# Performance work log

Measured on AMD Instinct MI355X. Metric: run time of the kernel, lower is better.

## Reference

```python
import jax, jax.numpy as jnp
import numpy as np
import math

L, C, H, FF, V, T, B = 12, 768, 12, 3072, 50257, 512, 4
D = C // H  # head dim = 64


def _layernorm(x, w, b, eps=1e-5):
    m = x.mean(-1, keepdims=True)
    v = ((x - m) ** 2).mean(-1, keepdims=True)
    return (x - m) / jnp.sqrt(v + eps) * w + b


def _gelu(x):
    # tanh-approximate GELU exactly as in the torch module
    return 0.5 * x * (1.0 + jnp.tanh(math.sqrt(2.0 / math.pi) * (x + 0.044715 * x ** 3)))


def setup_inputs() -> dict:
    key = jax.random.key(0)
    ks = jax.random.split(key, 12)
    std = 0.02
    proj_std = 0.02 / math.sqrt(2 * L)
    inp = {
        "idx": jax.random.randint(ks[0], (B, T), 0, V),
        "targets": jax.random.randint(ks[1], (B, T), 0, V),
        "wte": jax.random.normal(ks[2], (V, C), jnp.float32) * std,
        "wpe": jax.random.normal(ks[3], (T, C), jnp.float32) * std,
        "ln1_w": jnp.ones((L, C), jnp.float32),
        "ln1_b": jnp.zeros((L, C), jnp.float32),
        "attn_w": jax.random.normal(ks[4], (L, C, 3 * C), jnp.float32) * std,
        "attn_b": jnp.zeros((L, 3 * C), jnp.float32),
        "attnp_w": jax.random.normal(ks[5], (L, C, C), jnp.float32) * proj_std,
        "attnp_b": jnp.zeros((L, C), jnp.float32),
        "ln2_w": jnp.ones((L, C), jnp.float32),
        "ln2_b": jnp.zeros((L, C), jnp.float32),
        "fc_w": jax.random.normal(ks[6], (L, C, FF), jnp.float32) * std,
        "fc_b": jnp.zeros((L, FF), jnp.float32),
        "fcp_w": jax.random.normal(ks[7], (L, FF, C), jnp.float32) * proj_std,
        "fcp_b": jnp.zeros((L, C), jnp.float32),
        "lnf_w": jnp.ones((C,), jnp.float32),
        "lnf_b": jnp.zeros((C,), jnp.float32),
        "lm_w": jax.random.normal(ks[8], (C, V), jnp.float32) * std,  # lm_head.weight.T
    }
    return inp


def _gpt_forward(idx, targets, wte, wpe, ln1_w, ln1_b, attn_w, attn_b,
                 attnp_w, attnp_b, ln2_w, ln2_b, fc_w, fc_b, fcp_w, fcp_b,
                 lnf_w, lnf_b, lm_w):
    b, t = idx.shape
    x = wte[idx] + wpe[:t][None]  # [B,T,C]
    causal = jnp.tril(jnp.ones((t, t), bool))  # [T,T]
    neg_inf = jnp.float32(-jnp.inf)

    def block(x, p):
        l1w, l1b, aw, ab, pw, pb, l2w, l2b, fw, fb, qw, qb = p
        h = _layernorm(x, l1w, l1b)
        qkv = h @ aw + ab  # [B,T,3C]
        q, k, v = jnp.split(qkv, 3, axis=-1)
        q = q.reshape(b, t, H, D).transpose(0, 2, 1, 3)  # [B,H,T,D]
        k = k.reshape(b, t, H, D).transpose(0, 2, 1, 3)
        v = v.reshape(b, t, H, D).transpose(0, 2, 1, 3)
        att = jnp.einsum('bhqd,bhkd->bhqk', q, k) * (1.0 / math.sqrt(D))
        att = jnp.where(causal, att, neg_inf)
        att = jax.nn.softmax(att, axis=-1)
        y = jnp.einsum('bhqk,bhkd->bhqd', att, v)  # [B,H,T,D]
        y = y.transpose(0, 2, 1, 3).reshape(b, t, C)
        x = x + (y @ pw + pb)
        h2 = _layernorm(x, l2w, l2b)
        x = x + (_gelu(h2 @ fw + fb) @ qw + qb)
        return x, None

    params = (ln1_w, ln1_b, attn_w, attn_b, attnp_w, attnp_b,
              ln2_w, ln2_b, fc_w, fc_b, fcp_w, fcp_b)
    x, _ = jax.lax.scan(block, x, params)
    x = _layernorm(x, lnf_w, lnf_b)
    logits = x @ lm_w  # [B,T,V]

    # cross_entropy with ignore_index=-100
    logp = jax.nn.log_softmax(logits, axis=-1)
    tgt = targets.reshape(-1)
    valid = (tgt != -100)
    safe_tgt = jnp.where(valid, tgt, 0)
    nll = -jnp.take_along_axis(logp.reshape(-1, logits.shape[-1]),
                               safe_tgt[:, None], axis=1)[:, 0]
    loss = jnp.sum(nll * valid) / jnp.maximum(jnp.sum(valid), 1)
    return logits, loss


def reference(idx, targets, wte, wpe, ln1_w, ln1_b, attn_w, attn_b,
              attnp_w, attnp_b, ln2_w, ln2_b, fc_w, fc_b, fcp_w, fcp_b,
              lnf_w, lnf_b, lm_w):
    return _gpt_forward(idx, targets, wte, wpe, ln1_w, ln1_b, attn_w, attn_b,
                        attnp_w, attnp_b, ln2_w, ln2_b, fc_w, fc_b,
                        fcp_w, fcp_b, lnf_w, lnf_b, lm_w)
```

## Files before the change

kernel.cpp:

```cpp
#include <hip/hip_runtime.h>
#include <hip/hip_bf16.h>
#include <math.h>

#define L_ 12
#define C_ 768
#define H_ 12
#define FF_ 3072
#define V_ 50257
#define VP2_ 50432
#define T_ 512
#define B_ 4
#define D_ 64
#define M_ (B_*T_)
#define BH_ (B_*H_)
#define NPAN_LM 197

typedef __attribute__((ext_vector_type(8))) short short8;
typedef __attribute__((ext_vector_type(4))) float f32x4;
typedef __attribute__((ext_vector_type(8))) unsigned short us8;

__device__ __forceinline__ float bf2f(unsigned short u) {
    return __uint_as_float(((unsigned)u) << 16);
}
__device__ __forceinline__ unsigned short f2bf(float f) {
    unsigned u = __float_as_uint(f);
    unsigned r = u + 0x7fff + ((u >> 16) & 1);
    return (unsigned short)(r >> 16);
}

__device__ __forceinline__ void transpose_tile(
    const float* __restrict__ W, __hip_bfloat16* __restrict__ WT,
    int K, int N, int Npad, int bx, int by, int bz)
{
    __shared__ float tile[64][65];
    const float* Wl = W + (size_t)bz * K * N;
    __hip_bfloat16* WTl = WT + (size_t)bz * Npad * K;
    int k0 = by * 64, n0 = bx * 64;
    int tid = threadIdx.x;
    int tn = tid & 63, tk4 = tid >> 6;
#pragma unroll 4
    for (int i = 0; i < 16; ++i) {
        int k = tk4 * 16 + i;
        int n = n0 + tn;
        tile[k][tn] = (n < N) ? Wl[(size_t)(k0 + k) * N + n] : 0.f;
    }
    __syncthreads();
#pragma unroll
    for (int i = 0; i < 2; ++i) {
        int p = tid + i * 256;
        int n = p >> 3;
        int k8 = (p & 7) * 8;
        us8 v;
#pragma unroll
        for (int e = 0; e < 8; ++e) v[e] = f2bf(tile[k8 + e][n]);
        *(us8*)((unsigned short*)WTl + (size_t)(n0 + n) * K + k0 + k8) = v;
    }
}

__global__ __launch_bounds__(256) void transpose_all_kernel(
    const float* W0, __hip_bfloat16* T0,
    const float* W1, __hip_bfloat16* T1,
    const float* W2, __hip_bfloat16* T2,
    const float* W3, __hip_bfloat16* T3,
    const float* W4, __hip_bfloat16* T4)
{
    int bid = blockIdx.x;
    if (bid < 5184) {
        int bx = bid % 36, r = bid / 36;
        transpose_tile(W0, T0, C_, 3 * C_, 3 * C_, bx, r % 12, r / 12);
    } else if (bid < 6912) {
        int lb = bid - 5184;
        int bx = lb % 12, r = lb / 12;
        transpose_tile(W1, T1, C_, C_, C_, bx, r % 12, r / 12);
    } else if (bid < 13824) {
        int lb = bid - 6912;
        int bx = lb % 48, r = lb / 48;
        transpose_tile(W2, T2, C_, FF_, FF_, bx, r % 12, r / 12);
    } else if (bid < 20736) {
        int lb = bid - 13824;
        int bx = lb % 12, r = lb / 12;
        transpose_tile(W3, T3, FF_, C_, C_, bx, r % 48, r / 48);
    } else {
        int lb = bid - 20736;
        int bx = lb % 788, by = lb / 788;
        transpose_tile(W4, T4, C_, V_, VP2_, bx, by, 0);
    }
}

__global__ void embed_kernel(const int* __restrict__ idx, const float* __restrict__ wte,
                             const float* __restrict__ wpe, float* __restrict__ x, int total)
{
    int i = blockIdx.x * blockDim.x + threadIdx.x;
    if (i >= total) return;
    int c = i % C_;
    int row = i / C_;
    int t = row % T_;
    x[i] = wte[(size_t)idx[row] * C_ + c] + wpe[(size_t)t * C_ + c];
}

__global__ __launch_bounds__(256) void layernorm_kernel(
    const float* __restrict__ x, const float* __restrict__ w, const float* __restrict__ b,
    __hip_bfloat16* __restrict__ out)
{
    int row = blockIdx.x;
    int tid = threadIdx.x;
    const float* xr = x + (size_t)row * C_;
    float lx[3];
    float s = 0.f;
#pragma unroll
    for (int i = 0; i < 3; ++i) { lx[i] = xr[tid + i * 256]; s += lx[i]; }
    __shared__ float red[4];
    for (int off = 32; off > 0; off >>= 1) s += __shfl_down(s, off, 64);
    if ((tid & 63) == 0) red[tid >> 6] = s;
    __syncthreads();
    if (tid == 0) red[0] = red[0] + red[1] + red[2] + red[3];
    __syncthreads();
    float mean = red[0] * (1.f / (float)C_);
    __syncthreads();
    float v = 0.f;
#pragma unroll
    for (int i = 0; i < 3; ++i) { float d = lx[i] - mean; v += d * d; }
    for (int off = 32; off > 0; off >>= 1) v += __shfl_down(v, off, 64);
    if ((tid & 63) == 0) red[tid >> 6] = v;
    __syncthreads();
    if (tid == 0) red[0] = red[0] + red[1] + red[2] + red[3];
    __syncthreads();
    float rstd = rsqrtf(red[0] * (1.f / (float)C_) + 1e-5f);
#pragma unroll
    for (int i = 0; i < 3; ++i) {
        int c = tid + i * 256;
        ((unsigned short*)out)[(size_t)row * C_ + c] = f2bf((lx[i] - mean) * rstd * w[c] + b[c]);
    }
}

template<int MT, int NT, int WM, int WN, int BUFS, int SPLITK,
         int OUTBF, int GELU, int RESID, int LOSSP, int QKVPACK, int ATOMIC>
__global__ __launch_bounds__(64 * WM * WN) void mfma_gemm(
    const __hip_bfloat16* __restrict__ A,
    const __hip_bfloat16* __restrict__ Bt,
    const float* __restrict__ bias,
    const float* __restrict__ resid,
    void* __restrict__ Cout,
    int M, int N, int K, int NB,
    float* __restrict__ lpart, int NPAN,
    unsigned short* __restrict__ Qp, unsigned short* __restrict__ Kp,
    unsigned short* __restrict__ Vt)
{
    constexpr int NTHREADS = 64 * WM * WN;
    constexpr int MPAN = M_ / MT;
    constexpr int MFR = MT / (16 * WM);
    constexpr int AL = (MT * 4) / NTHREADS;
    constexpr int BL = (NT * 4) / NTHREADS;
    constexpr int LOADS = AL + BL;

    int nwg = NB * MPAN * SPLITK;
    int orig = blockIdx.x;
    int xcd = orig & 7;
    int q = nwg >> 3, rr_ = nwg & 7;
    int wgid = (xcd < rr_ ? xcd * (q + 1) : rr_ * (q + 1) + (xcd - rr_) * q) + (orig >> 3);
    int chunk = wgid / (NB * MPAN);
    int rem = wgid % (NB * MPAN);
    int npan = rem / MPAN, mpan = rem % MPAN;
    int m0 = mpan * MT, n0 = npan * NT;
    int KC = K / SPLITK;
    int kbase = chunk * KC;

    __shared__ __hip_bfloat16 As[BUFS][MT * 32];
    __shared__ __hip_bfloat16 Bs[BUFS][NT * 32];
    __shared__ float Lsum[WN][LOSSP ? MT : 1];
    int tid = threadIdx.x;
    int lane = tid & 63, w = tid >> 6;
    int wn = w % WN, wm = w / WN;
    int lrow = lane & 15, g = lane >> 4;
    f32x4 acc[MFR][4] = {};

    const __hip_bfloat16* Ab = A + (size_t)m0 * K + kbase;
    const __hip_bfloat16* Bb = Bt + (size_t)n0 * K + kbase;

    auto stage = [&](int buf, int k0) {
#pragma unroll
        for (int i = 0; i < AL; ++i) {
            int c = tid + i * NTHREADS;
            int row = c >> 2, s = c & 3;
            int l = (s - (row >> 1)) & 3;
            __builtin_amdgcn_global_load_lds(
                (const __attribute__((address_space(1))) void*)(Ab + (size_t)row * K + k0 + l * 8),
                (__attribute__((address_space(3))) void*)(&As[buf][c * 8]), 16, 0, 0);
        }
#pragma unroll
        for (int i = 0; i < BL; ++i) {
            int c = tid + i * NTHREADS;
            int row = c >> 2, s = c & 3;
            int l = (s - (row >> 1)) & 3;
            __builtin_amdgcn_global_load_lds(
                (const __attribute__((address_space(1))) void*)(Bb + (size_t)row * K + k0 + l * 8),
                (__attribute__((address_space(3))) void*)(&Bs[buf][c * 8]), 16, 0, 0);
        }
    };
    auto do_tile = [&](int buf) {
        short8 a[MFR], b[4];
#pragma unroll
        for (int i = 0; i < MFR; ++i) {
            int row = wm * (MT / WM) + i * 16 + lrow;
            int s = (g + (row >> 1)) & 3;
            a[i] = *(const short8*)&As[buf][row * 32 + s * 8];
        }
#pragma unroll
        for (int j = 0; j < 4; ++j) {
            int row = wn * 64 + j * 16 + lrow;
            int s = (g + (row >> 1)) & 3;
            b[j] = *(const short8*)&Bs[buf][row * 32 + s * 8];
        }
        asm volatile("s_waitcnt lgkmcnt(0)" ::: "memory");
        __builtin_amdgcn_sched_barrier(0);
        __builtin_amdgcn_s_setprio(1);
#pragma unroll
        for (int i = 0; i < MFR; ++i)
#pragma unroll
            for (int j = 0; j < 4; ++j)
                acc[i][j] = __builtin_amdgcn_mfma_f32_16x16x32_bf16(a[i], b[j], acc[i][j], 0, 0, 0);
        __builtin_amdgcn_s_setprio(0);
    };

    int nk = KC >> 5;
#pragma unroll
    for (int i = 0; i < BUFS - 1; ++i) stage(i, i << 5);
    for (int t = 0; t < nk; ++t) {
        int ahead = nk - 1 - t;
        if (ahead > BUFS - 2) ahead = BUFS - 2;
        if (ahead == 1) {
            if constexpr (LOADS == 3) asm volatile("s_waitcnt vmcnt(3)" ::: "memory");
            else                      asm volatile("s_waitcnt vmcnt(4)" ::: "memory");
        } else if (ahead >= 2) {
            if constexpr (LOADS == 3) asm volatile("s_waitcnt vmcnt(6)" ::: "memory");
            else                      asm volatile("s_waitcnt vmcnt(8)" ::: "memory");
        } else {
            asm volatile("s_waitcnt vmcnt(0)" ::: "memory");
        }
        __builtin_amdgcn_s_barrier();
        if (t + BUFS - 1 < nk) stage((t + BUFS - 1) % BUFS, (t + BUFS - 1) << 5);
        do_tile(t % BUFS);
    }

    int r0 = g * 4;
#pragma unroll
    for (int i = 0; i < MFR; ++i) {
#pragma unroll
        for (int j = 0; j < 4; ++j) {
            int col = n0 + wn * 64 + j * 16 + lrow;
            if (col >= N) continue;
            float bv = (bias && (SPLITK == 1 || chunk == 0)) ? bias[col] : 0.f;
#pragma unroll
            for (int r = 0; r < 4; ++r) {
                int row = m0 + wm * (MT / WM) + i * 16 + r0 + r;
                float v = acc[i][j][r] + bv;
                if (GELU) {
                    float t = 0.7978845608028654f * (v + 0.044715f * v * v * v);
                    v = 0.5f * v * (1.f + tanhf(t));
                }
                if (RESID) v += resid[(size_t)row * N + col];
                if (ATOMIC) {
                    atomicAdd(&((float*)Cout)[(size_t)row * N + col], v);
                } else if (QKVPACK) {
                    int bb = row >> 9, tt = row & (T_ - 1);
                    int which = col / 768;
                    int cc = col - which * 768;
                    int hh = cc >> 6, d = cc & 63;
                    size_t bh = (size_t)bb * H_ + hh;
                    unsigned short u = f2bf(v);
                    if (which == 0)      Qp[(bh * T_ + tt) * 64 + d] = u;
                    else if (which == 1) Kp[(bh * T_ + tt) * 64 + d] = u;
                    else                 Vt[(bh * 64 + d) * T_ + tt] = u;
                } else if (OUTBF) {
                    ((unsigned short*)Cout)[(size_t)row * N + col] = f2bf(v);
                } else {
                    ((float*)Cout)[(size_t)row * N + col] = v;
                }
            }
        }
    }
    if (LOSSP) {
#pragma unroll
        for (int i = 0; i < MFR; ++i) {
#pragma unroll
            for (int r = 0; r < 4; ++r) {
                float ss = 0.f;
#pragma unroll
                for (int j = 0; j < 4; ++j) {
                    int col = n0 + wn * 64 + j * 16 + lrow;
                    if (col < V_) ss += __expf(acc[i][j][r]);
                }
#pragma unroll
                for (int d2 = 1; d2 < 16; d2 <<= 1) ss += __shfl_xor(ss, d2, 64);
                if ((lane & 15) == 0) {
                    int rloc = wm * (MT / WM) + i * 16 + g * 4 + r;
                    Lsum[wn][rloc] = ss;
                }
            }
        }
        __syncthreads();
        if (tid < MT) {
            float ss = Lsum[0][tid];
#pragma unroll
            for (int ww = 1; ww < WN; ++ww) ss += Lsum[ww][tid];
            lpart[(size_t)(m0 + tid) * NPAN + npan] = ss;
        }
    }
}

__global__ __launch_bounds__(256) void flash_attn_kernel(
    const unsigned short* __restrict__ Qp, const unsigned short* __restrict__ Kp,
    const unsigned short* __restrict__ Vt, unsigned short* __restrict__ y)
{
    int bid = blockIdx.x;
    int xcd = bid & 7;
    int s_ = bid >> 3;
    int bh = xcd * 6 + (s_ % 6);
    int qg = 7 - s_ / 6;
    int b = bh / H_, h = bh % H_;
    int tid = threadIdx.x;
    int w = tid >> 6;
    int lane = tid & 63;
    int c = lane & 15, g = lane >> 4;
    int q0 = (qg * 4 + w) * 16;

    const unsigned short* Qb = Qp + ((size_t)bh * T_ + q0) * 64;
    const unsigned short* Kb = Kp + (size_t)bh * T_ * 64;
    const unsigned short* Vb = Vt + (size_t)bh * 64 * T_;

    short8 qf0 = *(const short8*)(Qb + (size_t)c * 64 + g * 8);
    short8 qf1 = *(const short8*)(Qb + (size_t)c * 64 + 32 + g * 8);

    f32x4 o[4] = {};
    float mrow[4], lrow[4];
#pragma unroll
    for (int r = 0; r < 4; ++r) { mrow[r] = -1e30f; lrow[r] = 0.f; }

    __shared__ unsigned short P_lds[4][16 * 40];

    int ntiles = q0 / 32 + 1;
    for (int t = 0; t < ntiles; ++t) {
        int kv0 = t * 32;
        f32x4 s[2] = {};
        __builtin_amdgcn_s_setprio(1);
#pragma unroll
        for (int tt = 0; tt < 2; ++tt) {
            const unsigned short* Kt = Kb + (size_t)(kv0 + tt * 16 + c) * 64;
            short8 b0 = *(const short8*)(Kt + g * 8);
            short8 b1 = *(const short8*)(Kt + 32 + g * 8);
            s[tt] = __builtin_amdgcn_mfma_f32_16x16x32_bf16(qf0, b0, s[tt], 0, 0, 0);
            s[tt] = __builtin_amdgcn_mfma_f32_16x16x32_bf16(qf1, b1, s[tt], 0, 0, 0);
        }
        __builtin_amdgcn_s_setprio(0);
        if (kv0 + 32 > q0) {
#pragma unroll
            for (int tt = 0; tt < 2; ++tt)
#pragma unroll
                for (int r = 0; r < 4; ++r) {
                    int kv = kv0 + tt * 16 + c;
                    int qq = q0 + g * 4 + r;
                    float v = s[tt][r] * 0.125f;
                    s[tt][r] = (kv <= qq) ? v : -1e30f;
                }
        } else {
#pragma unroll
            for (int tt = 0; tt < 2; ++tt)
#pragma unroll
                for (int r = 0; r < 4; ++r) s[tt][r] *= 0.125f;
        }
        float pmax[4];
#pragma unroll
        for (int r = 0; r < 4; ++r) pmax[r] = fmaxf(s[0][r], s[1][r]);
#pragma unroll
        for (int d2 = 1; d2 < 16; d2 <<= 1)
#pragma unroll
            for (int r = 0; r < 4; ++r) pmax[r] = fmaxf(pmax[r], __shfl_xor(pmax[r], d2, 64));
        float scl[4], psum[4];
#pragma unroll
        for (int r = 0; r < 4; ++r) {
            float mnew = fmaxf(mrow[r], pmax[r]);
            scl[r] = __expf(mrow[r] - mnew);
            mrow[r] = mnew;
            s[0][r] = __expf(s[0][r] - mnew);
            s[1][r] = __expf(s[1][r] - mnew);
            psum[r] = s[0][r] + s[1][r];
        }
#pragma unroll
        for (int d2 = 1; d2 < 16; d2 <<= 1)
#pragma unroll
            for (int r = 0; r < 4; ++r) psum[r] += __shfl_xor(psum[r], d2, 64);
#pragma unroll
        for (int r = 0; r < 4; ++r) lrow[r] = lrow[r] * scl[r] + psum[r];
#pragma unroll
        for (int j = 0; j < 4; ++j)
#pragma unroll
            for (int r = 0; r < 4; ++r) o[j][r] *= scl[r];
#pragma unroll
        for (int tt = 0; tt < 2; ++tt)
#pragma unroll
            for (int r = 0; r < 4; ++r)
                P_lds[w][(g * 4 + r) * 40 + tt * 16 + c] = f2bf(s[tt][r]);
        asm volatile("s_waitcnt lgkmcnt(0)" ::: "memory");
        __builtin_amdgcn_sched_barrier(0);
        short8 pf = *(const short8*)&P_lds[w][c * 40 + g * 8];
        asm volatile("s_waitcnt lgkmcnt(0)" ::: "memory");
        asm volatile("" ::: "memory");
        __builtin_amdgcn_s_setprio(1);
#pragma unroll
        for (int j = 0; j < 4; ++j) {
            short8 vf = *(const short8*)(Vb + (size_t)(j * 16 + c) * T_ + kv0 + g * 8);
            o[j] = __builtin_amdgcn_mfma_f32_16x16x32_bf16(pf, vf, o[j], 0, 0, 0);
        }
        __builtin_amdgcn_s_setprio(0);
    }
    unsigned short* yb = y + ((size_t)(b * T_ + q0)) * C_ + h * 64;
#pragma unroll
    for (int r = 0; r < 4; ++r) {
        float inv = 1.f / lrow[r];
#pragma unroll
        for (int j = 0; j < 4; ++j)
            yb[(size_t)(g * 4 + r) * C_ + j * 16 + c] = f2bf(o[j][r] * inv);
    }
}

__global__ __launch_bounds__(256) void loss_reduce_kernel(
    const float* __restrict__ lpart, const float* __restrict__ logits,
    const int* __restrict__ targets, float* __restrict__ rnll, int NPAN)
{
    int row = blockIdx.x;
    const float* pp = lpart + (size_t)row * NPAN;
    int tid = threadIdx.x;
    float s = 0.f;
    for (int j = tid; j < NPAN; j += 256) s += pp[j];
    for (int off = 32; off > 0; off >>= 1) s += __shfl_down(s, off, 64);
    __shared__ float rs[4];
    if ((tid & 63) == 0) rs[tid >> 6] = s;
    __syncthreads();
    if (tid == 0) {
        float S = rs[0] + rs[1] + rs[2] + rs[3];
        int t = targets[row];
        if (t != -100) {
            rnll[row] = -(logits[(size_t)row * V_ + t] - logf(S));
            rnll[M_ + row] = 1.f;
        } else {
            rnll[row] = 0.f;
            rnll[M_ + row] = 0.f;
        }
    }
}

__global__ __launch_bounds__(256) void finalize_loss(
    const float* __restrict__ rnll, float* __restrict__ out)
{
    int tid = threadIdx.x;
    float sn = 0.f, sc = 0.f;
    for (int j = tid; j < M_; j += 256) { sn += rnll[j]; sc += rnll[M_ + j]; }
    for (int off = 32; off > 0; off >>= 1) {
        sn += __shfl_down(sn, off, 64);
        sc += __shfl_down(sc, off, 64);
    }
    __shared__ float rn[4], rc[4];
    if ((tid & 63) == 0) { rn[tid >> 6] = sn; rc[tid >> 6] = sc; }
    __syncthreads();
    if (tid == 0) {
        float N = rn[0] + rn[1] + rn[2] + rn[3];
        float Cn = rc[0] + rc[1] + rc[2] + rc[3];
        out[0] = N / fmaxf(Cn, 1.f);
    }
}

extern "C" void kernel_launch(void* const* d_in, const int* in_sizes, int n_in,
                              void* d_out, int out_size, void* d_ws, size_t ws_size,
                              hipStream_t stream)
{
    const int*   idx     = (const int*)d_in[0];
    const int*   targets = (const int*)d_in[1];
    const float* wte     = (const float*)d_in[2];
    const float* wpe     = (const float*)d_in[3];
    const float* ln1_w   = (const float*)d_in[4];
    const float* ln1_b   = (const float*)d_in[5];
    const float* attn_w  = (const float*)d_in[6];
    const float* attn_b  = (const float*)d_in[7];
    const float* attnp_w = (const float*)d_in[8];
    const float* attnp_b = (const float*)d_in[9];
    const float* ln2_w   = (const float*)d_in[10];
    const float* ln2_b   = (const float*)d_in[11];
    const float* fc_w    = (const float*)d_in[12];
    const float* fc_b    = (const float*)d_in[13];
    const float* fcp_w   = (const float*)d_in[14];
    const float* fcp_b   = (const float*)d_in[15];
    const float* lnf_w   = (const float*)d_in[16];
    const float* lnf_b   = (const float*)d_in[17];
    const float* lm_w    = (const float*)d_in[18];

    float* logits = (float*)d_out;
    float* loss   = logits + (size_t)M_ * V_;

    char* p = (char*)d_ws;
    __hip_bfloat16* aw_t = (__hip_bfloat16*)p; p += (size_t)L_ * 3 * C_ * C_ * 2;
    __hip_bfloat16* pw_t = (__hip_bfloat16*)p; p += (size_t)L_ * C_ * C_ * 2;
    __hip_bfloat16* fw_t = (__hip_bfloat16*)p; p += (size_t)L_ * FF_ * C_ * 2;
    __hip_bfloat16* qw_t = (__hip_bfloat16*)p; p += (size_t)L_ * C_ * FF_ * 2;
    __hip_bfloat16* lm_t = (__hip_bfloat16*)p; p += (size_t)VP2_ * C_ * 2;
    float*          x    = (float*)p;          p += (size_t)M_ * C_ * 4;
    __hip_bfloat16* h    = (__hip_bfloat16*)p; p += (size_t)M_ * C_ * 2;
    __hip_bfloat16* y    = (__hip_bfloat16*)p; p += (size_t)M_ * C_ * 2;
    __hip_bfloat16* ff   = (__hip_bfloat16*)p; p += (size_t)M_ * FF_ * 2;
    unsigned short* Qp   = (unsigned short*)p; p += (size_t)BH_ * T_ * 64 * 2;
    unsigned short* Kp   = (unsigned short*)p; p += (size_t)BH_ * T_ * 64 * 2;
    unsigned short* Vt   = (unsigned short*)p; p += (size_t)BH_ * 64 * T_ * 2;
    float*          lpart= (float*)p;          p += (size_t)M_ * NPAN_LM * 4;
    float*          rnll = (float*)p;          p += (size_t)2 * M_ * 4;

    transpose_all_kernel<<<30192, 256, 0, stream>>>(
        attn_w, aw_t, attnp_w, pw_t, fc_w, fw_t, fcp_w, qw_t, lm_w, lm_t);

    {
        int total = M_ * C_;
        embed_kernel<<<(total + 255) / 256, 256, 0, stream>>>(idx, wte, wpe, x, total);
    }

    for (int l = 0; l < L_; ++l) {
        const float* l1w = ln1_w + (size_t)l * C_;
        const float* l1b = ln1_b + (size_t)l * C_;
        const __hip_bfloat16* aw = aw_t + (size_t)l * 3 * C_ * C_;
        const float* ab  = attn_b + (size_t)l * 3 * C_;
        const __hip_bfloat16* pw = pw_t + (size_t)l * C_ * C_;
        const float* pb  = attnp_b + (size_t)l * C_;
        const float* l2w = ln2_w + (size_t)l * C_;
        const float* l2b = ln2_b + (size_t)l * C_;
        const __hip_bfloat16* fw = fw_t + (size_t)l * FF_ * C_;
        const float* fb  = fc_b + (size_t)l * FF_;
        const __hip_bfloat16* qw = qw_t + (size_t)l * C_ * FF_;
        const float* qb  = fcp_b + (size_t)l * C_;

        layernorm_kernel<<<M_, 256, 0, stream>>>(x, l1w, l1b, h);
        mfma_gemm<128, 128, 2, 2, 3, 1, 0, 0, 0, 0, 1, 0><<<18 * 16, 256, 0, stream>>>(
            h, aw, ab, nullptr, nullptr, M_, 3 * C_, C_, 18, nullptr, 0, Qp, Kp, Vt);
        flash_attn_kernel<<<384, 256, 0, stream>>>(Qp, Kp, Vt, (unsigned short*)y);
        mfma_gemm<64, 128, 2, 2, 3, 2, 0, 0, 0, 0, 0, 1><<<6 * 32 * 2, 256, 0, stream>>>(
            y, pw, pb, nullptr, x, M_, C_, C_, 6, nullptr, 0, nullptr, nullptr, nullptr);
        layernorm_kernel<<<M_, 256, 0, stream>>>(x, l2w, l2b, h);
        mfma_gemm<128, 128, 2, 2, 3, 1, 1, 1, 0, 0, 0, 0><<<24 * 16, 256, 0, stream>>>(
            h, fw, fb, nullptr, ff, M_, FF_, C_, 24, nullptr, 0, nullptr, nullptr, nullptr);
        mfma_gemm<64, 128, 2, 2, 3, 4, 0, 0, 0, 0, 0, 1><<<6 * 32 * 4, 256, 0, stream>>>(
            ff, qw, qb, nullptr, x, M_, C_, FF_, 6, nullptr, 0, nullptr, nullptr, nullptr);
    }

    layernorm_kernel<<<M_, 256, 0, stream>>>(x, lnf_w, lnf_b, h);
    mfma_gemm<128, 256, 2, 4, 3, 1, 0, 0, 0, 1, 0, 0><<<NPAN_LM * 16, 512, 0, stream>>>(
        h, lm_t, nullptr, nullptr, logits, M_, V_, C_, NPAN_LM, lpart, NPAN_LM,
        nullptr, nullptr, nullptr);

    loss_reduce_kernel<<<M_, 256, 0, stream>>>(lpart, logits, targets, rnll, NPAN_LM);
    finalize_loss<<<1, 256, 0, stream>>>(rnll, loss);
}
```

Before: 2.468 ms.

## Use wave-per-row layernorm, vectorized QKV epilogue, and prefetched QK tiles in attention

LayerNorm now gives each wavefront one row and uses float4 loads and stores with shuffle-only reductions, which removes the shared-memory barriers. The QKV GEMM epilogue gets its own branch that writes V transposed with 4-wide vector stores and hoists the Q/K/V selection out of the inner loop. Flash attention computes the next tile's QK^T MFMAs before doing softmax on the current tile, so K loads and MFMA overlap with the exp work. The cost is higher register pressure in the attention kernel.

```diff
diff --git a/kernel.cpp b/kernel.cpp
--- a/kernel.cpp
+++ b/kernel.cpp
@@ -18,6 +18,7 @@
 typedef __attribute__((ext_vector_type(8))) short short8;
 typedef __attribute__((ext_vector_type(4))) float f32x4;
 typedef __attribute__((ext_vector_type(8))) unsigned short us8;
+typedef __attribute__((ext_vector_type(4))) unsigned short us4;
 
 __device__ __forceinline__ float bf2f(unsigned short u) {
     return __uint_as_float(((unsigned)u) << 16);
@@ -102,34 +103,38 @@
     const float* __restrict__ x, const float* __restrict__ w, const float* __restrict__ b,
     __hip_bfloat16* __restrict__ out)
 {
-    int row = blockIdx.x;
-    int tid = threadIdx.x;
+    int wv = threadIdx.x >> 6, lane = threadIdx.x & 63;
+    int row = blockIdx.x * 4 + wv;
     const float* xr = x + (size_t)row * C_;
-    float lx[3];
+    f32x4 v[3];
     float s = 0.f;
 #pragma unroll
-    for (int i = 0; i < 3; ++i) { lx[i] = xr[tid + i * 256]; s += lx[i]; }
-    __shared__ float red[4];
-    for (int off = 32; off > 0; off >>= 1) s += __shfl_down(s, off, 64);
-    if ((tid & 63) == 0) red[tid >> 6] = s;
-    __syncthreads();
-    if (tid == 0) red[0] = red[0] + red[1] + red[2] + red[3];
-    __syncthreads();
-    float mean = red[0] * (1.f / (float)C_);
-    __syncthreads();
-    float v = 0.f;
-#pragma unroll
-    for (int i = 0; i < 3; ++i) { float d = lx[i] - mean; v += d * d; }
-    for (int off = 32; off > 0; off >>= 1) v += __shfl_down(v, off, 64);
-    if ((tid & 63) == 0) red[tid >> 6] = v;
-    __syncthreads();
-    if (tid == 0) red[0] = red[0] + red[1] + red[2] + red[3];
-    __syncthreads();
-    float rstd = rsqrtf(red[0] * (1.f / (float)C_) + 1e-5f);
-#pragma unroll
-    for (int i = 0; i < 3; ++i) {
-        int c = tid + i * 256;
-        ((unsigned short*)out)[(size_t)row * C_ + c] = f2bf((lx[i] - mean) * rstd * w[c] + b[c]);
+    for (int j = 0; j < 3; ++j) {
+        v[j] = *(const f32x4*)(xr + j * 256 + lane * 4);
+        s += v[j][0] + v[j][1] + v[j][2] + v[j][3];
+    }
+#pragma unroll
+    for (int off = 32; off; off >>= 1) s += __shfl_xor(s, off, 64);
+    float mean = s * (1.f / (float)C_);
+    float var = 0.f;
+#pragma unroll
+    for (int j = 0; j < 3; ++j)
+#pragma unroll
+        for (int e = 0; e < 4; ++e) { float d = v[j][e] - mean; var += d * d; }
+#pragma unroll
+    for (int off = 32; off; off >>= 1) var += __shfl_xor(var, off, 64);
+    float rstd = rsqrtf(var * (1.f / (float)C_) + 1e-5f);
+    unsigned short* o = (unsigned short*)out + (size_t)row * C_;
+#pragma unroll
+    for (int j = 0; j < 3; ++j) {
+        int c0 = j * 256 + lane * 4;
+        f32x4 wv4 = *(const f32x4*)(w + c0);
+        f32x4 bv4 = *(const f32x4*)(b + c0);
+        us4 u;
+#pragma unroll
+        for (int e = 0; e < 4; ++e)
+            u[e] = f2bf((v[j][e] - mean) * rstd * wv4[e] + bv4[e]);
+        *(us4*)(o + c0) = u;
     }
 }
 
@@ -243,38 +248,56 @@
     }
 
     int r0 = g * 4;
-#pragma unroll
-    for (int i = 0; i < MFR; ++i) {
-#pragma unroll
-        for (int j = 0; j < 4; ++j) {
-            int col = n0 + wn * 64 + j * 16 + lrow;
-            if (col >= N) continue;
-            float bv = (bias && (SPLITK == 1 || chunk == 0)) ? bias[col] : 0.f;
-#pragma unroll
-            for (int r = 0; r < 4; ++r) {
-                int row = m0 + wm * (MT / WM) + i * 16 + r0 + r;
-                float v = acc[i][j][r] + bv;
-                if (GELU) {
-                    float t = 0.7978845608028654f * (v + 0.044715f * v * v * v);
-                    v = 0.5f * v * (1.f + tanhf(t));
+    if (QKVPACK) {
+        int which = n0 / 768;
+#pragma unroll
+        for (int i = 0; i < MFR; ++i) {
+#pragma unroll
+            for (int j = 0; j < 4; ++j) {
+                int col = n0 + wn * 64 + j * 16 + lrow;
+                float bv = bias ? bias[col] : 0.f;
+                int cc = col - which * 768;
+                int hh = cc >> 6, d = cc & 63;
+                int row0 = m0 + wm * (MT / WM) + i * 16 + r0;
+                int bb = row0 >> 9, tt0 = row0 & (T_ - 1);
+                size_t bh = (size_t)bb * H_ + hh;
+                if (which == 2) {
+                    us4 u;
+#pragma unroll
+                    for (int r = 0; r < 4; ++r) u[r] = f2bf(acc[i][j][r] + bv);
+                    *(us4*)(Vt + (bh * 64 + d) * T_ + tt0) = u;
+                } else {
+                    unsigned short* dst = (which == 0) ? Qp : Kp;
+#pragma unroll
+                    for (int r = 0; r < 4; ++r)
+                        dst[(bh * T_ + tt0 + r) * 64 + d] = f2bf(acc[i][j][r] + bv);
                 }
-                if (RESID) v += resid[(size_t)row * N + col];
-                if (ATOMIC) {
-                    atomicAdd(&((float*)Cout)[(size_t)row * N + col], v);
-                } else if (QKVPACK) {
-                    int bb = row >> 9, tt = row & (T_ - 1);
-                    int which = col / 768;
-                    int cc = col - which * 768;
-                    int hh = cc >> 6, d = cc & 63;
-                    size_t bh = (size_t)bb * H_ + hh;
-                    unsigned short u = f2bf(v);
-                    if (which == 0)      Qp[(bh * T_ + tt) * 64 + d] = u;
-                    else if (which == 1) Kp[(bh * T_ + tt) * 64 + d] = u;
-                    else                 Vt[(bh * 64 + d) * T_ + tt] = u;
-                } else if (OUTBF) {
-                    ((unsigned short*)Cout)[(size_t)row * N + col] = f2bf(v);
-                } else {
-                    ((float*)Cout)[(size_t)row * N + col] = v;
+            }
+        }
+    } else {
+#pragma unroll
+        for (int i = 0; i < MFR; ++i) {
+#pragma unroll
+            for (int j = 0; j < 4; ++j) {
+                int col = n0 + wn * 64 + j * 16 + lrow;
+                if (col >= N) continue;
+                float bv = (bias && (SPLITK == 1 || chunk == 0)) ? bias[col] : 0.f;
+#pragma unroll
+                for (int r = 0; r < 4; ++r) {
+                    int row = m0 + wm * (MT / WM) + i * 16 + r0 + r;
+                    float v = acc[i][j][r] + bv;
+                    if (GELU) {
+                        float t = 0.7978845608028654f * (v + 0.044715f * v * v * v);
+                        v = 0.5f * v * (1.f + tanhf(t));
+                    }
+                    if (RESID) v += resid[(size_t)row * N + col];
+                    if (ATOMIC) {
+                        atomicAdd(&((float*)Cout)[(size_t)row * N + col], v);
+                    } else if (OUTBF) {
+                        ((unsigned short*)Cout)[(size_t)row * N + col] = f2bf(v);
+                    } else {
+                        ((float*)Cout)[(size_t)row * N + col] = v;
+                    }
                 }
             }
         }
@@ -338,39 +361,46 @@
 
     __shared__ unsigned short P_lds[4][16 * 40];
 
+    auto qk_tile = [&](int kv0, f32x4& t0, f32x4& t1) {
+        t0 = (f32x4){0.f, 0.f, 0.f, 0.f};
+        t1 = (f32x4){0.f, 0.f, 0.f, 0.f};
+        const unsigned short* Kt0 = Kb + (size_t)(kv0 + c) * 64;
+        short8 b0 = *(const short8*)(Kt0 + g * 8);
+        short8 b1 = *(const short8*)(Kt0 + 32 + g * 8);
+        const unsigned short* Kt1 = Kb + (size_t)(kv0 + 16 + c) * 64;
+        short8 b2 = *(const short8*)(Kt1 + g * 8);
+        short8 b3 = *(const short8*)(Kt1 + 32 + g * 8);
+        __builtin_amdgcn_s_setprio(1);
+        t0 = __builtin_amdgcn_mfma_f32_16x16x32_bf16(qf0, b0, t0, 0, 0, 0);
+        t0 = __builtin_amdgcn_mfma_f32_16x16x32_bf16(qf1, b1, t0, 0, 0, 0);
+        t1 = __builtin_amdgcn_mfma_f32_16x16x32_bf16(qf0, b2, t1, 0, 0, 0);
+        t1 = __builtin_amdgcn_mfma_f32_16x16x32_bf16(qf1, b3, t1, 0, 0, 0);
+        __builtin_amdgcn_s_setprio(0);
+    };
+
     int ntiles = q0 / 32 + 1;
+    f32x4 sN0, sN1;
+    qk_tile(0, sN0, sN1);
     for (int t = 0; t < ntiles; ++t) {
         int kv0 = t * 32;
-        f32x4 s[2] = {};
-        __builtin_amdgcn_s_setprio(1);
-#pragma unroll
-        for (int tt = 0; tt < 2; ++tt) {
-            const unsigned short* Kt = Kb + (size_t)(kv0 + tt * 16 + c) * 64;
-            short8 b0 = *(const short8*)(Kt + g * 8);
-            short8 b1 = *(const short8*)(Kt + 32 + g * 8);
-            s[tt] = __builtin_amdgcn_mfma_f32_16x16x32_bf16(qf0, b0, s[tt], 0, 0, 0);
-            s[tt] = __builtin_amdgcn_mfma_f32_16x16x32_bf16(qf1, b1, s[tt], 0, 0, 0);
-        }
-        __builtin_amdgcn_s_setprio(0);
+        f32x4 s0 = sN0, s1 = sN1;
+        if (t + 1 < ntiles) qk_tile(kv0 + 32, sN0, sN1);
         if (kv0 + 32 > q0) {
 #pragma unroll
-            for (int tt = 0; tt < 2; ++tt)
-#pragma unroll
-                for (int r = 0; r < 4; ++r) {
-                    int kv = kv0 + tt * 16 + c;
-                    int qq = q0 + g * 4 + r;
-                    float v = s[tt][r] * 0.125f;
-                    s[tt][r] = (kv <= qq) ? v : -1e30f;
-                }
+            for (int r = 0; r < 4; ++r) {
+                int qq = q0 + g * 4 + r;
+                float v0 = s0[r] * 0.125f;
+                float v1 = s1[r] * 0.125f;
+                s0[r] = (kv0 + c <= qq) ? v0 : -1e30f;
+                s1[r] = (kv0 + 16 + c <= qq) ? v1 : -1e30f;
+            }
         } else {
 #pragma unroll
-            for (int tt = 0; tt < 2; ++tt)
-#pragma unroll
-                for (int r = 0; r < 4; ++r) s[tt][r] *= 0.125f;
+            for (int r = 0; r < 4; ++r) { s0[r] *= 0.125f; s1[r] *= 0.125f; }
         }
         float pmax[4];
 #pragma unroll
-        for (int r = 0; r < 4; ++r) pmax[r] = fmaxf(s[0][r], s[1][r]);
+        for (int r = 0; r < 4; ++r) pmax[r] = fmaxf(s0[r], s1[r]);
 #pragma unroll
         for (int d2 = 1; d2 < 16; d2 <<= 1)
 #pragma unroll
@@ -381,9 +411,9 @@
             float mnew = fmaxf(mrow[r], pmax[r]);
             scl[r] = __expf(mrow[r] - mnew);
             mrow[r] = mnew;
-            s[0][r] = __expf(s[0][r] - mnew);
-            s[1][r] = __expf(s[1][r] - mnew);
-            psum[r] = s[0][r] + s[1][r];
+            s0[r] = __expf(s0[r] - mnew);
+            s1[r] = __expf(s1[r] - mnew);
+            psum[r] = s0[r] + s1[r];
         }
 #pragma unroll
         for (int d2 = 1; d2 < 16; d2 <<= 1)
@@ -396,10 +426,10 @@
 #pragma unroll
             for (int r = 0; r < 4; ++r) o[j][r] *= scl[r];
 #pragma unroll
-        for (int tt = 0; tt < 2; ++tt)
-#pragma unroll
-            for (int r = 0; r < 4; ++r)
-                P_lds[w][(g * 4 + r) * 40 + tt * 16 + c] = f2bf(s[tt][r]);
+        for (int r = 0; r < 4; ++r) {
+            P_lds[w][(g * 4 + r) * 40 + c] = f2bf(s0[r]);
+            P_lds[w][(g * 4 + r) * 40 + 16 + c] = f2bf(s1[r]);
+        }
         asm volatile("s_waitcnt lgkmcnt(0)" ::: "memory");
         __builtin_amdgcn_sched_barrier(0);
         short8 pf = *(const short8*)&P_lds[w][c * 40 + g * 8];
@@ -534,20 +564,20 @@
         const __hip_bfloat16* qw = qw_t + (size_t)l * C_ * FF_;
         const float* qb  = fcp_b + (size_t)l * C_;
 
-        layernorm_kernel<<<M_, 256, 0, stream>>>(x, l1w, l1b, h);
+        layernorm_kernel<<<M_ / 4, 256, 0, stream>>>(x, l1w, l1b, h);
         mfma_gemm<128, 128, 2, 2, 3, 1, 0, 0, 0, 0, 1, 0><<<18 * 16, 256, 0, stream>>>(
             h, aw, ab, nullptr, nullptr, M_, 3 * C_, C_, 18, nullptr, 0, Qp, Kp, Vt);
         flash_attn_kernel<<<384, 256, 0, stream>>>(Qp, Kp, Vt, (unsigned short*)y);
         mfma_gemm<64, 128, 2, 2, 3, 2, 0, 0, 0, 0, 0, 1><<<6 * 32 * 2, 256, 0, stream>>>(
             y, pw, pb, nullptr, x, M_, C_, C_, 6, nullptr, 0, nullptr, nullptr, nullptr);
-        layernorm_kernel<<<M_, 256, 0, stream>>>(x, l2w, l2b, h);
+        layernorm_kernel<<<M_ / 4, 256, 0, stream>>>(x, l2w, l2b, h);
         mfma_gemm<128, 128, 2, 2, 3, 1, 1, 1, 0, 0, 0, 0><<<24 * 16, 256, 0, stream>>>(
             h, fw, fb, nullptr, ff, M_, FF_, C_, 24, nullptr, 0, nullptr, nullptr, nullptr);
         mfma_gemm<64, 128, 2, 2, 3, 4, 0, 0, 0, 0, 0, 1><<<6 * 32 * 4, 256, 0, stream>>>(
             ff, qw, qb, nullptr, x, M_, C_, FF_, 6, nullptr, 0, nullptr, nullptr, nullptr);
     }
 
-    layernorm_kernel<<<M_, 256, 0, stream>>>(x, lnf_w, lnf_b, h);
+    layernorm_kernel<<<M_ / 4, 256, 0, stream>>>(x, lnf_w, lnf_b, h);
     mfma_gemm<128, 256, 2, 4, 3, 1, 0, 0, 0, 1, 0, 0><<<NPAN_LM * 16, 512, 0, stream>>>(
         h, lm_t, nullptr, nullptr, logits, M_, V_, C_, NPAN_LM, lpart, NPAN_LM,
         nullptr, nullptr, nullptr);
```

Measured after the change: 2.288 ms. 1.08x faster.
